# Kernel optimization log

Hardware: AMD Instinct MI355X
Metric: run time of the kernel (lower is better)

The kernel has to match this reference:

```python
import jax, jax.numpy as jnp
import numpy as np

B, C, N = 8, 256, 4096

def setup_inputs() -> dict:
    key = jax.random.key(0)
    k1, k2, k3 = jax.random.split(key, 3)
    pts_feat = jax.random.normal(k1, (B, C, N), dtype=jnp.float32)
    # Conv1d(channels, channels, 1, bias=False) weight is [C_out, C_in, 1] -> store as [C_out, C_in]
    scale = 1.0 / np.sqrt(C)
    Wq = jax.random.uniform(k2, (C, C), dtype=jnp.float32, minval=-scale, maxval=scale)
    Wk = jax.random.uniform(k3, (C, C), dtype=jnp.float32, minval=-scale, maxval=scale)
    return {"pts_feat": pts_feat, "Wq": Wq, "Wk": Wk}

def reference(pts_feat, Wq, Wk):
    # 1x1 conv == channel-wise matmul. x_q: [B, N, C], x_k: [B, C, N]
    x_q = jnp.einsum('bcn,dc->bnd', pts_feat, Wq)
    x_k = jnp.einsum('bcn,dc->bdn', pts_feat, Wk)
    logits = jnp.einsum('bnc,bcm->bnm', x_q, x_k)          # [B, N, N]
    attn = jax.nn.softmax(logits, axis=-1)
    attn = attn / (1e-8 + attn.sum(axis=-1, keepdims=True))
    # torch.einsum('bnn,bnc->bnc', attn, feat) takes the DIAGONAL of attn
    # and scales each point's raw feature vector by it (no contraction).
    diag = jnp.diagonal(attn, axis1=1, axis2=2)            # [B, N]
    x_attn = pts_feat * diag[:, None, :]                   # [B, C, N]
    return x_attn
```

## Files before the change

### kernel.cpp

```cpp
#include <hip/hip_runtime.h>
#include <hip/hip_bf16.h>
#include <cstdint>

#define B_ 8
#define C_ 256
#define N_ 4096

typedef __bf16 bf16;
typedef __bf16 bf16x8 __attribute__((ext_vector_type(8)));
typedef float f32x4 __attribute__((ext_vector_type(4)));
typedef unsigned int u32;

__device__ __forceinline__ void async_ld16(const void* g, void* l) {
  __builtin_amdgcn_global_load_lds(
      (const __attribute__((address_space(1))) void*)g,
      (__attribute__((address_space(3))) void*)l, 16, 0, 0);
}

__device__ __forceinline__ float bh2f(unsigned short u) {
  union { u32 i; float f; } x; x.i = ((u32)u) << 16; return x.f;
}
__device__ __forceinline__ unsigned short f2bh(float f) {
  union { float f; u32 i; } x; x.f = f;
  u32 i = x.i + 0x7fffu + ((x.i >> 16) & 1u);
  return (unsigned short)(i >> 16);
}

__device__ __forceinline__ bool wave_sniff_fp32(const unsigned short* p) {
  int l = threadIdx.x & 63;
  unsigned short u = p[2 * l];
  int e = (u >> 7) & 0xff;
  unsigned long long m = __ballot(e >= 112 && e <= 142);
  return __popcll(m) < 32;
}

__global__ __launch_bounds__(256) void k_mt(const void* __restrict__ Wqv,
                                            const void* __restrict__ Wkv,
                                            unsigned short* __restrict__ Mt) {
  __shared__ float wkcol[C_];
  int t = threadIdx.x;
  bool fq = wave_sniff_fp32((const unsigned short*)Wqv);
  bool fk = wave_sniff_fp32((const unsigned short*)Wkv);
  int d = blockIdx.x, c = t;
  if (fk)
    wkcol[c] = ((const float*)Wkv)[c * C_ + d];
  else
    wkcol[c] = bh2f(((const unsigned short*)Wkv)[c * C_ + d]);
  __syncthreads();
  float acc = 0.f;
  if (fq) {
    for (int e0 = 0; e0 < C_; e0 += 16) {
      float wq[16];
#pragma unroll
      for (int j = 0; j < 16; ++j) wq[j] = ((const float*)Wqv)[(e0 + j) * C_ + c];
#pragma unroll
      for (int j = 0; j < 16; ++j) acc += wkcol[e0 + j] * wq[j];
    }
  } else {
    for (int e0 = 0; e0 < C_; e0 += 16) {
      float wq[16];
#pragma unroll
      for (int j = 0; j < 16; ++j) wq[j] = bh2f(((const unsigned short*)Wqv)[(e0 + j) * C_ + c]);
#pragma unroll
      for (int j = 0; j < 16; ++j) acc += wkcol[e0 + j] * wq[j];
    }
  }
  Mt[(size_t)d * C_ + c] = f2bh(acc * 1.44269504f);
}

__global__ __launch_bounds__(256, 3) void k_tp(const void* __restrict__ Fv,
                                               const bf16* __restrict__ Mt,
                                               unsigned short* __restrict__ Ft,
                                               bf16* __restrict__ G) {
  __shared__ unsigned short tile[128 * 72];
  __shared__ bf16 As[8 * 64 * 32];
  int n0 = blockIdx.x * 64;
  int b = blockIdx.y;
  int t = threadIdx.x;
  bool f32 = wave_sniff_fp32((const unsigned short*)Fv);

#pragma unroll
  for (int hp = 0; hp < 2; ++hp) {
    if (hp) __syncthreads();
#pragma unroll
    for (int p = 0; p < 4; ++p) {
      int cl = (t >> 3) + 32 * p;
      int n8 = t & 7;
      size_t off = (size_t)(b * C_ + hp * 128 + cl) * N_ + n0 + n8 * 8;
      u32 o[4];
      if (f32) {
        const float* src = (const float*)Fv + off;
        float4 v0 = *(const float4*)(src);
        float4 v1 = *(const float4*)(src + 4);
        o[0] = ((u32)f2bh(v0.y) << 16) | f2bh(v0.x);
        o[1] = ((u32)f2bh(v0.w) << 16) | f2bh(v0.z);
        o[2] = ((u32)f2bh(v1.y) << 16) | f2bh(v1.x);
        o[3] = ((u32)f2bh(v1.w) << 16) | f2bh(v1.z);
      } else {
        uint4 v = *(const uint4*)((const unsigned short*)Fv + off);
        o[0] = v.x; o[1] = v.y; o[2] = v.z; o[3] = v.w;
      }
      uint4 ov; ov.x = o[0]; ov.y = o[1]; ov.z = o[2]; ov.w = o[3];
      int slot = (n8 + cl + (cl >> 3)) & 7;
      *(uint4*)(tile + cl * 72 + slot * 8) = ov;
    }
    __syncthreads();
#pragma unroll
    for (int p = 0; p < 2; ++p) {
      int flat = p * 256 + t;
      int np = flat >> 4, oc = flat & 15;
      int n = 2 * np, n8 = np >> 2, no = n & 7;
      u32 on0[4], on1[4];
#pragma unroll
      for (int k = 0; k < 4; ++k) {
        int row0 = oc * 8 + 2 * k, row1 = row0 + 1;
        int s0 = (n8 + row0 + oc) & 7;
        int s1 = (n8 + row1 + oc) & 7;
        u32 lo = *(const u32*)(tile + row0 * 72 + s0 * 8 + no);
        u32 hi = *(const u32*)(tile + row1 * 72 + s1 * 8 + no);
        on0[k] = ((hi & 0xffffu) << 16) | (lo & 0xffffu);
        on1[k] = (hi & 0xffff0000u) | (lo >> 16);
      }
      uint4 v0; v0.x = on0[0]; v0.y = on0[1]; v0.z = on0[2]; v0.w = on0[3];
      uint4 v1; v1.x = on1[0]; v1.y = on1[1]; v1.z = on1[2]; v1.w = on1[3];
      *(uint4*)(Ft + ((size_t)(b * N_ + n0 + n)) * C_ + hp * 128 + oc * 8) = v0;
      *(uint4*)(Ft + ((size_t)(b * N_ + n0 + n + 1)) * C_ + hp * 128 + oc * 8) = v1;
      int gc = hp * 16 + oc;
      int kc = gc >> 2, col8 = gc & 3, sw = np & 3;
      *(uint4*)((unsigned short*)As + kc * 2048 + n * 32 + (col8 ^ sw) * 8) = v0;
      *(uint4*)((unsigned short*)As + kc * 2048 + (n + 1) * 32 + (col8 ^ sw) * 8) = v1;
    }
  }
  __syncthreads();

  int w = t >> 6, l = t & 63, lr = l & 15, lq = l >> 4;
  int wn = w * 32;
  int rchunk = (lq ^ ((lr >> 1) & 3)) * 8;
  const size_t fbase = (size_t)b * N_ * C_;
#pragma unroll
  for (int jp = 0; jp < 2; ++jp) {
    int d0 = jp * 128;
    bf16x8 bb[2][8];
#pragma unroll
    for (int j = 0; j < 2; ++j)
#pragma unroll
      for (int kc = 0; kc < 8; ++kc)
        bb[j][kc] = *(const bf16x8*)(Mt + (size_t)(d0 + wn + 16 * j + lr) * C_ + kc * 32 + lq * 8);
    f32x4 acc[4][2] = {};
#pragma unroll
    for (int kc = 0; kc < 8; ++kc) {
#pragma unroll
      for (int i = 0; i < 4; ++i) {
        bf16x8 a = *(const bf16x8*)(As + kc * 2048 + (16 * i + lr) * 32 + rchunk);
#pragma unroll
        for (int j = 0; j < 2; ++j)
          acc[i][j] = __builtin_amdgcn_mfma_f32_16x16x32_bf16(a, bb[j][kc], acc[i][j], 0, 0, 0);
      }
    }
    __syncthreads();
    unsigned short* Cs = (unsigned short*)tile;
#pragma unroll
    for (int i = 0; i < 4; ++i)
#pragma unroll
      for (int j = 0; j < 2; ++j)
#pragma unroll
        for (int r = 0; r < 4; ++r)
          Cs[(16 * i + lq * 4 + r) * 136 + wn + 16 * j + lr] = f2bh(acc[i][j][r]);
    __syncthreads();
#pragma unroll
    for (int p = 0; p < 4; ++p) {
      int idx = p * 256 + t;
      int row = idx >> 4, c8 = idx & 15;
      uint4 v = *(const uint4*)(Cs + row * 136 + c8 * 8);
      *(uint4*)(G + fbase + (size_t)(n0 + row) * C_ + d0 + c8 * 8) = v;
    }
  }
}

__global__ __launch_bounds__(256, 4) void k_attn(const bf16* __restrict__ G,
                                                 const bf16* __restrict__ Ft,
                                                 float* __restrict__ snn,
                                                 float* __restrict__ lsum) {
  __shared__ bf16 Ks[2][32 * 256];
  int bid = blockIdx.x;
  int b = bid & 7, q = (bid >> 3) & 3, ntile = bid >> 5;
  int n0 = ntile * 128;
  int t = threadIdx.x, w = t >> 6, l = t & 63;
  int lr = l & 15, lq = l >> 4;
  int wrow = w * 32;
  const size_t gbase = (size_t)b * N_ * C_;

  bf16x8 a[2][8];
#pragma unroll
  for (int i = 0; i < 2; ++i)
#pragma unroll
    for (int kc = 0; kc < 8; ++kc)
      a[i][kc] = *(const bf16x8*)(G + gbase + (size_t)(n0 + wrow + 16 * i + lr) * C_ + kc * 32 + lq * 8);

  float part[8];
#pragma unroll
  for (int s = 0; s < 8; ++s) part[s] = 0.f;

  int m_base = q * 1024;
  bool has_diag = (q == (ntile >> 3));
  int dbase = (ntile & 7) * 4;

  int soff[4];
#pragma unroll
  for (int p = 0; p < 4; ++p) {
    int flat = p * 256 + t;
    int kc = flat >> 7;
    int r = (flat >> 2) & 31;
    int col8 = flat & 3;
    soff[p] = r * C_ + kc * 32 + ((col8 ^ ((r >> 1) & 3)) * 8);
  }
  int rchunk = (lq ^ ((lr >> 1) & 3)) * 8;

#pragma unroll
  for (int p = 0; p < 4; ++p)
    async_ld16(Ft + gbase + (size_t)m_base * C_ + soff[p],
               (bf16*)Ks + (p * 256 + t) * 8);
  asm volatile("s_waitcnt vmcnt(0)" ::: "memory");
  __builtin_amdgcn_s_barrier();

  for (int it = 0; it < 32; ++it) {
    int cur = it & 1;
    if (it < 31) {
      int m0 = m_base + (it + 1) * 32;
#pragma unroll
      for (int p = 0; p < 4; ++p)
        async_ld16(Ft + gbase + (size_t)m0 * C_ + soff[p],
                   (bf16*)Ks + (cur ^ 1) * 8192 + (p * 256 + t) * 8);
    }
    const bf16* ks = (const bf16*)Ks + cur * 8192;
    f32x4 acc[2][2] = {};
#pragma unroll
    for (int kc = 0; kc < 8; ++kc) {
      bf16x8 b0 = *(const bf16x8*)(ks + kc * 1024 + lr * 32 + rchunk);
      bf16x8 b1 = *(const bf16x8*)(ks + kc * 1024 + (16 + lr) * 32 + rchunk);
      acc[0][0] = __builtin_amdgcn_mfma_f32_16x16x32_bf16(a[0][kc], b0, acc[0][0], 0, 0, 0);
      acc[1][0] = __builtin_amdgcn_mfma_f32_16x16x32_bf16(a[1][kc], b0, acc[1][0], 0, 0, 0);
      acc[0][1] = __builtin_amdgcn_mfma_f32_16x16x32_bf16(a[0][kc], b1, acc[0][1], 0, 0, 0);
      acc[1][1] = __builtin_amdgcn_mfma_f32_16x16x32_bf16(a[1][kc], b1, acc[1][1], 0, 0, 0);
    }
    bool dit = has_diag && ((it >> 2) == (ntile & 7));
#pragma unroll
    for (int i = 0; i < 2; ++i)
#pragma unroll
      for (int j = 0; j < 2; ++j)
#pragma unroll
        for (int r = 0; r < 4; ++r) {
          float e = __builtin_amdgcn_exp2f(acc[i][j][r]);
          part[i * 4 + r] += e;
          if (dit) {
            int rloc = wrow + 16 * i + lq * 4 + r;
            int cloc = 16 * j + lr;
            if ((it - dbase) * 32 + cloc == rloc) snn[b * N_ + n0 + rloc] = e;
          }
        }
    if (it < 31) {
      asm volatile("s_waitcnt vmcnt(0)" ::: "memory");
      __builtin_amdgcn_s_barrier();
    }
  }

#pragma unroll
  for (int s = 0; s < 8; ++s) {
    float v = part[s];
    v += __shfl_xor(v, 1);
    v += __shfl_xor(v, 2);
    v += __shfl_xor(v, 4);
    v += __shfl_xor(v, 8);
    part[s] = v;
  }
  if (lr == 0) {
#pragma unroll
    for (int i = 0; i < 2; ++i)
#pragma unroll
      for (int r = 0; r < 4; ++r)
        lsum[((size_t)q * B_ + b) * N_ + n0 + wrow + 16 * i + lq * 4 + r] = part[i * 4 + r];
  }
}

__global__ __launch_bounds__(256) void k_scale(const void* __restrict__ Fv,
                                               const float* __restrict__ snn,
                                               const float* __restrict__ lsum,
                                               void* __restrict__ Outv) {
  __shared__ __align__(16) float dd_lds[64];
  bool f32 = wave_sniff_fp32((const unsigned short*)Fv);
  int bid = blockIdx.x;
  int b = bid >> 8;
  int cq = (bid >> 6) & 3;
  int n0 = (bid & 63) * 64;
  int t = threadIdx.x;
  if (t < 64) {
    int n = n0 + t;
    float s = snn[(size_t)b * N_ + n];
    float ls = 0.f;
#pragma unroll
    for (int p = 0; p < 4; ++p) ls += lsum[((size_t)p * B_ + b) * N_ + n];
    dd_lds[t] = s / (ls * (1.0f + 1e-8f));
  }
  __syncthreads();
  const size_t fb = (size_t)b * C_ * N_ + (size_t)cq * 64 * N_;
  if (f32) {
    const float* F = (const float*)Fv;
    float* O = (float*)Outv;
#pragma unroll
    for (int p = 0; p < 4; ++p) {
      int idx = p * 256 + t;
      int row = idx >> 4, ch = idx & 15;
      size_t off = fb + (size_t)row * N_ + n0 + ch * 4;
      float4 v = *(const float4*)(F + off);
      float4 d = *(const float4*)(&dd_lds[ch * 4]);
      float4 o;
      o.x = v.x * d.x; o.y = v.y * d.y; o.z = v.z * d.z; o.w = v.w * d.w;
      *(float4*)(O + off) = o;
    }
  } else {
    const unsigned short* F = (const unsigned short*)Fv;
    unsigned short* O = (unsigned short*)Outv;
#pragma unroll
    for (int p = 0; p < 2; ++p) {
      int idx = p * 256 + t;
      int row = idx >> 3, ch = idx & 7;
      size_t off = fb + (size_t)row * N_ + n0 + ch * 8;
      uint4 v = *(const uint4*)(F + off);
      u32 vv[4] = {v.x, v.y, v.z, v.w};
      u32 o[4];
#pragma unroll
      for (int k = 0; k < 4; ++k) {
        float lo = bh2f((unsigned short)(vv[k] & 0xffffu)) * dd_lds[ch * 8 + 2 * k];
        float hi = bh2f((unsigned short)(vv[k] >> 16)) * dd_lds[ch * 8 + 2 * k + 1];
        o[k] = ((u32)f2bh(hi) << 16) | f2bh(lo);
      }
      uint4 ov; ov.x = o[0]; ov.y = o[1]; ov.z = o[2]; ov.w = o[3];
      *(uint4*)(O + off) = ov;
    }
  }
}

extern "C" void kernel_launch(void* const* d_in, const int* in_sizes, int n_in,
                              void* d_out, int out_size, void* d_ws, size_t ws_size,
                              hipStream_t stream) {
  (void)in_sizes; (void)n_in; (void)out_size; (void)ws_size;
  const void* F = d_in[0];
  const void* Wq = d_in[1];
  const void* Wk = d_in[2];
  char* ws = (char*)d_ws;
  bf16* Ft = (bf16*)(ws);
  bf16* G = (bf16*)(ws + (16u << 20));
  char* tail = ws + (32u << 20);
  float* snn = (float*)(tail);
  float* lsum = (float*)(tail + 131072);
  bf16* Mt = (bf16*)(tail + 131072 + 524288);

  k_mt<<<256, 256, 0, stream>>>(Wq, Wk, (unsigned short*)Mt);
  k_tp<<<dim3(N_ / 64, B_), 256, 0, stream>>>(F, Mt, (unsigned short*)Ft, G);
  k_attn<<<1024, 256, 0, stream>>>(G, Ft, snn, lsum);
  k_scale<<<2048, 256, 0, stream>>>(F, snn, lsum, d_out);
}
```

Baseline: 171.6 us.

## Fuse scale epilogue into attention kernel via last-block atomic ticket

Drops the separate k_scale launch. Each k_attn block takes an atomic ticket per (ntile, batch) group, and the last of the four q-split blocks computes the diagonal scale factors and writes the scaled output for its 128 points across all 256 channels. The counters are reset in k_mt. This saves a launch and its tail, but the output pass now runs on only 256 blocks, with each doing a large serial loop at the end, which could lower memory parallelism.

```diff
diff --git a/kernel.cpp b/kernel.cpp
--- a/kernel.cpp
+++ b/kernel.cpp
@@ -36,9 +36,11 @@
 
 __global__ __launch_bounds__(256) void k_mt(const void* __restrict__ Wqv,
                                             const void* __restrict__ Wkv,
-                                            unsigned short* __restrict__ Mt) {
+                                            unsigned short* __restrict__ Mt,
+                                            int* __restrict__ cnt) {
   __shared__ float wkcol[C_];
   int t = threadIdx.x;
+  if (t == 0) cnt[blockIdx.x] = 0;
   bool fq = wave_sniff_fp32((const unsigned short*)Wqv);
   bool fk = wave_sniff_fp32((const unsigned short*)Wkv);
   int d = blockIdx.x, c = t;
@@ -180,8 +182,13 @@
 __global__ __launch_bounds__(256, 4) void k_attn(const bf16* __restrict__ G,
                                                  const bf16* __restrict__ Ft,
                                                  float* __restrict__ snn,
-                                                 float* __restrict__ lsum) {
+                                                 float* __restrict__ lsum,
+                                                 const void* __restrict__ Fv,
+                                                 void* __restrict__ Outv,
+                                                 int* __restrict__ cnt) {
   __shared__ bf16 Ks[2][32 * 256];
+  __shared__ int s_ticket;
+  __shared__ __align__(16) float dd_lds[128];
   int bid = blockIdx.x;
   int b = bid & 7, q = (bid >> 3) & 3, ntile = bid >> 5;
   int n0 = ntile * 128;
@@ -280,20 +287,17 @@
       for (int r = 0; r < 4; ++r)
         lsum[((size_t)q * B_ + b) * N_ + n0 + wrow + 16 * i + lq * 4 + r] = part[i * 4 + r];
   }
-}
-
-__global__ __launch_bounds__(256) void k_scale(const void* __restrict__ Fv,
-                                               const float* __restrict__ snn,
-                                               const float* __restrict__ lsum,
-                                               void* __restrict__ Outv) {
-  __shared__ __align__(16) float dd_lds[64];
-  bool f32 = wave_sniff_fp32((const unsigned short*)Fv);
-  int bid = blockIdx.x;
-  int b = bid >> 8;
-  int cq = (bid >> 6) & 3;
-  int n0 = (bid & 63) * 64;
-  int t = threadIdx.x;
-  if (t < 64) {
+
+  __syncthreads();
+  if (t == 0) {
+    __threadfence();
+    s_ticket = atomicAdd(&cnt[ntile * 8 + b], 1);
+  }
+  __syncthreads();
+  if (s_ticket != 3) return;
+  __threadfence();
+  bool f32o = wave_sniff_fp32((const unsigned short*)Fv);
+  if (t < 128) {
     int n = n0 + t;
     float s = snn[(size_t)b * N_ + n];
     float ls = 0.f;
@@ -302,15 +306,15 @@
     dd_lds[t] = s / (ls * (1.0f + 1e-8f));
   }
   __syncthreads();
-  const size_t fb = (size_t)b * C_ * N_ + (size_t)cq * 64 * N_;
-  if (f32) {
+  const size_t fb = (size_t)b * C_ * N_;
+  if (f32o) {
     const float* F = (const float*)Fv;
     float* O = (float*)Outv;
 #pragma unroll
-    for (int p = 0; p < 4; ++p) {
+    for (int p = 0; p < 32; ++p) {
       int idx = p * 256 + t;
-      int row = idx >> 4, ch = idx & 15;
-      size_t off = fb + (size_t)row * N_ + n0 + ch * 4;
+      int c = idx >> 5, ch = idx & 31;
+      size_t off = fb + (size_t)c * N_ + n0 + ch * 4;
       float4 v = *(const float4*)(F + off);
       float4 d = *(const float4*)(&dd_lds[ch * 4]);
       float4 o;
@@ -321,10 +325,10 @@
     const unsigned short* F = (const unsigned short*)Fv;
     unsigned short* O = (unsigned short*)Outv;
 #pragma unroll
-    for (int p = 0; p < 2; ++p) {
+    for (int p = 0; p < 16; ++p) {
       int idx = p * 256 + t;
-      int row = idx >> 3, ch = idx & 7;
-      size_t off = fb + (size_t)row * N_ + n0 + ch * 8;
+      int c = idx >> 4, ch = idx & 15;
+      size_t off = fb + (size_t)c * N_ + n0 + ch * 8;
       uint4 v = *(const uint4*)(F + off);
       u32 vv[4] = {v.x, v.y, v.z, v.w};
       u32 o[4];
@@ -354,9 +358,9 @@
   float* snn = (float*)(tail);
   float* lsum = (float*)(tail + 131072);
   bf16* Mt = (bf16*)(tail + 131072 + 524288);
-
-  k_mt<<<256, 256, 0, stream>>>(Wq, Wk, (unsigned short*)Mt);
+  int* cnt = (int*)(tail + 131072 + 524288 + 131072);
+
+  k_mt<<<256, 256, 0, stream>>>(Wq, Wk, (unsigned short*)Mt, cnt);
   k_tp<<<dim3(N_ / 64, B_), 256, 0, stream>>>(F, Mt, (unsigned short*)Ft, G);
-  k_attn<<<1024, 256, 0, stream>>>(G, Ft, snn, lsum);
-  k_scale<<<2048, 256, 0, stream>>>(F, snn, lsum, d_out);
-}
+  k_attn<<<1024, 256, 0, stream>>>(G, Ft, snn, lsum, F, d_out, cnt);
+}
```

Measured after the change: 223.8 us. 1.3x slower.

## Enlarge attention row tile, deepen K prefetch ring, widen scale blocks

Applied to the files above, without the earlier changes.

The attention kernel now gives each block 256 query rows instead of 128, so each wave holds 64 rows of A in registers and each K tile loaded into LDS is reused by twice as many MFMAs. The LDS ring grows to four stages with a three-tile-ahead async prefetch and partial vmcnt waits, so the barrier no longer waits for the next load. MFMA issue is wrapped in s_setprio, and the diagonal extraction is simplified. The scale kernel now processes all channels per block with 512 blocks instead of 2048. The cost is higher register and LDS pressure (launch bounds drop to 2) and fewer blocks to spread across CUs.

```diff
diff --git a/kernel.cpp b/kernel.cpp
--- a/kernel.cpp
+++ b/kernel.cpp
@@ -177,33 +177,33 @@
   }
 }
 
-__global__ __launch_bounds__(256, 4) void k_attn(const bf16* __restrict__ G,
+__global__ __launch_bounds__(256, 2) void k_attn(const bf16* __restrict__ G,
                                                  const bf16* __restrict__ Ft,
                                                  float* __restrict__ snn,
                                                  float* __restrict__ lsum) {
-  __shared__ bf16 Ks[2][32 * 256];
+  __shared__ bf16 Ks[4][32 * 256];
   int bid = blockIdx.x;
   int b = bid & 7, q = (bid >> 3) & 3, ntile = bid >> 5;
-  int n0 = ntile * 128;
+  int n0 = ntile * 256;
   int t = threadIdx.x, w = t >> 6, l = t & 63;
   int lr = l & 15, lq = l >> 4;
-  int wrow = w * 32;
+  int wrow = w * 64;
   const size_t gbase = (size_t)b * N_ * C_;
 
-  bf16x8 a[2][8];
-#pragma unroll
-  for (int i = 0; i < 2; ++i)
+  bf16x8 a[32];
+#pragma unroll
+  for (int i = 0; i < 4; ++i)
 #pragma unroll
     for (int kc = 0; kc < 8; ++kc)
-      a[i][kc] = *(const bf16x8*)(G + gbase + (size_t)(n0 + wrow + 16 * i + lr) * C_ + kc * 32 + lq * 8);
-
-  float part[8];
-#pragma unroll
-  for (int s = 0; s < 8; ++s) part[s] = 0.f;
+      a[i * 8 + kc] = *(const bf16x8*)(G + gbase + (size_t)(n0 + wrow + 16 * i + lr) * C_ + kc * 32 + lq * 8);
+
+  float part[16];
+#pragma unroll
+  for (int s = 0; s < 16; ++s) part[s] = 0.f;
 
   int m_base = q * 1024;
-  bool has_diag = (q == (ntile >> 3));
-  int dbase = (ntile & 7) * 4;
+  bool has_diag = (q == (ntile >> 2));
+  int dbase = (ntile & 3) * 8;
 
   int soff[4];
 #pragma unroll
@@ -217,55 +217,61 @@
   int rchunk = (lq ^ ((lr >> 1) & 3)) * 8;
 
 #pragma unroll
-  for (int p = 0; p < 4; ++p)
-    async_ld16(Ft + gbase + (size_t)m_base * C_ + soff[p],
-               (bf16*)Ks + (p * 256 + t) * 8);
-  asm volatile("s_waitcnt vmcnt(0)" ::: "memory");
-  __builtin_amdgcn_s_barrier();
+  for (int s = 0; s < 3; ++s)
+#pragma unroll
+    for (int p = 0; p < 4; ++p)
+      async_ld16(Ft + gbase + (size_t)(m_base + s * 32) * C_ + soff[p],
+                 (bf16*)Ks + s * 8192 + (p * 256 + t) * 8);
 
   for (int it = 0; it < 32; ++it) {
-    int cur = it & 1;
-    if (it < 31) {
-      int m0 = m_base + (it + 1) * 32;
+    if (it <= 29) {
+      asm volatile("s_waitcnt vmcnt(8)" ::: "memory");
+    } else if (it == 30) {
+      asm volatile("s_waitcnt vmcnt(4)" ::: "memory");
+    } else {
+      asm volatile("s_waitcnt vmcnt(0)" ::: "memory");
+    }
+    __builtin_amdgcn_s_barrier();
+    if (it <= 28) {
+      int m0 = m_base + (it + 3) * 32;
+      bf16* dst = (bf16*)Ks + ((it + 3) & 3) * 8192;
 #pragma unroll
       for (int p = 0; p < 4; ++p)
-        async_ld16(Ft + gbase + (size_t)m0 * C_ + soff[p],
-                   (bf16*)Ks + (cur ^ 1) * 8192 + (p * 256 + t) * 8);
-    }
-    const bf16* ks = (const bf16*)Ks + cur * 8192;
-    f32x4 acc[2][2] = {};
+        async_ld16(Ft + gbase + (size_t)m0 * C_ + soff[p], dst + (p * 256 + t) * 8);
+    }
+
+    const bf16* ks = (const bf16*)Ks + (it & 3) * 8192;
+    f32x4 acc[8] = {};
+    __builtin_amdgcn_s_setprio(1);
 #pragma unroll
     for (int kc = 0; kc < 8; ++kc) {
       bf16x8 b0 = *(const bf16x8*)(ks + kc * 1024 + lr * 32 + rchunk);
       bf16x8 b1 = *(const bf16x8*)(ks + kc * 1024 + (16 + lr) * 32 + rchunk);
-      acc[0][0] = __builtin_amdgcn_mfma_f32_16x16x32_bf16(a[0][kc], b0, acc[0][0], 0, 0, 0);
-      acc[1][0] = __builtin_amdgcn_mfma_f32_16x16x32_bf16(a[1][kc], b0, acc[1][0], 0, 0, 0);
-      acc[0][1] = __builtin_amdgcn_mfma_f32_16x16x32_bf16(a[0][kc], b1, acc[0][1], 0, 0, 0);
-      acc[1][1] = __builtin_amdgcn_mfma_f32_16x16x32_bf16(a[1][kc], b1, acc[1][1], 0, 0, 0);
-    }
-    bool dit = has_diag && ((it >> 2) == (ntile & 7));
-#pragma unroll
-    for (int i = 0; i < 2; ++i)
+#pragma unroll
+      for (int i = 0; i < 4; ++i) {
+        acc[i * 2 + 0] = __builtin_amdgcn_mfma_f32_16x16x32_bf16(a[i * 8 + kc], b0, acc[i * 2 + 0], 0, 0, 0);
+        acc[i * 2 + 1] = __builtin_amdgcn_mfma_f32_16x16x32_bf16(a[i * 8 + kc], b1, acc[i * 2 + 1], 0, 0, 0);
+      }
+    }
+    __builtin_amdgcn_s_setprio(0);
+
+#pragma unroll
+    for (int i = 0; i < 4; ++i) {
+      bool dit = has_diag && (it == dbase + 2 * w + (i >> 1));
 #pragma unroll
       for (int j = 0; j < 2; ++j)
 #pragma unroll
         for (int r = 0; r < 4; ++r) {
-          float e = __builtin_amdgcn_exp2f(acc[i][j][r]);
+          float e = __builtin_amdgcn_exp2f(acc[i * 2 + j][r]);
           part[i * 4 + r] += e;
-          if (dit) {
-            int rloc = wrow + 16 * i + lq * 4 + r;
-            int cloc = 16 * j + lr;
-            if ((it - dbase) * 32 + cloc == rloc) snn[b * N_ + n0 + rloc] = e;
-          }
+          if (dit && j == (i & 1) && lr == lq * 4 + r)
+            snn[b * N_ + n0 + wrow + 16 * i + lq * 4 + r] = e;
         }
-    if (it < 31) {
-      asm volatile("s_waitcnt vmcnt(0)" ::: "memory");
-      __builtin_amdgcn_s_barrier();
-    }
-  }
-
-#pragma unroll
-  for (int s = 0; s < 8; ++s) {
+    }
+  }
+
+#pragma unroll
+  for (int s = 0; s < 16; ++s) {
     float v = part[s];
     v += __shfl_xor(v, 1);
     v += __shfl_xor(v, 2);
@@ -275,7 +281,7 @@
   }
   if (lr == 0) {
 #pragma unroll
-    for (int i = 0; i < 2; ++i)
+    for (int i = 0; i < 4; ++i)
 #pragma unroll
       for (int r = 0; r < 4; ++r)
         lsum[((size_t)q * B_ + b) * N_ + n0 + wrow + 16 * i + lq * 4 + r] = part[i * 4 + r];
@@ -289,9 +295,7 @@
   __shared__ __align__(16) float dd_lds[64];
   bool f32 = wave_sniff_fp32((const unsigned short*)Fv);
   int bid = blockIdx.x;
-  int b = bid >> 8;
-  int cq = (bid >> 6) & 3;
-  int n0 = (bid & 63) * 64;
+  int b = bid >> 6, n0 = (bid & 63) * 64;
   int t = threadIdx.x;
   if (t < 64) {
     int n = n0 + t;
@@ -302,15 +306,15 @@
     dd_lds[t] = s / (ls * (1.0f + 1e-8f));
   }
   __syncthreads();
-  const size_t fb = (size_t)b * C_ * N_ + (size_t)cq * 64 * N_;
+  const size_t fb = (size_t)b * C_ * N_;
   if (f32) {
     const float* F = (const float*)Fv;
     float* O = (float*)Outv;
 #pragma unroll
-    for (int p = 0; p < 4; ++p) {
+    for (int p = 0; p < 16; ++p) {
       int idx = p * 256 + t;
-      int row = idx >> 4, ch = idx & 15;
-      size_t off = fb + (size_t)row * N_ + n0 + ch * 4;
+      int c = idx >> 4, ch = idx & 15;
+      size_t off = fb + (size_t)c * N_ + n0 + ch * 4;
       float4 v = *(const float4*)(F + off);
       float4 d = *(const float4*)(&dd_lds[ch * 4]);
       float4 o;
@@ -321,10 +325,10 @@
     const unsigned short* F = (const unsigned short*)Fv;
     unsigned short* O = (unsigned short*)Outv;
 #pragma unroll
-    for (int p = 0; p < 2; ++p) {
+    for (int p = 0; p < 8; ++p) {
       int idx = p * 256 + t;
-      int row = idx >> 3, ch = idx & 7;
-      size_t off = fb + (size_t)row * N_ + n0 + ch * 8;
+      int c = idx >> 3, ch = idx & 7;
+      size_t off = fb + (size_t)c * N_ + n0 + ch * 8;
       uint4 v = *(const uint4*)(F + off);
       u32 vv[4] = {v.x, v.y, v.z, v.w};
       u32 o[4];
@@ -357,6 +361,6 @@
 
   k_mt<<<256, 256, 0, stream>>>(Wq, Wk, (unsigned short*)Mt);
   k_tp<<<dim3(N_ / 64, B_), 256, 0, stream>>>(F, Mt, (unsigned short*)Ft, G);
-  k_attn<<<1024, 256, 0, stream>>>(G, Ft, snn, lsum);
-  k_scale<<<2048, 256, 0, stream>>>(F, snn, lsum, d_out);
-}
+  k_attn<<<512, 256, 0, stream>>>(G, Ft, snn, lsum);
+  k_scale<<<512, 256, 0, stream>>>(F, snn, lsum, d_out);
+}
```

Result: faster. 167.7 us (-2.2%).
